# Kernel tuning notes

Hardware: AMD Instinct MI355X
Metric: run time of the kernel (lower is better)

## Reference

```python
import jax, jax.numpy as jnp
import numpy as np

N_NODES = 50000
N_EDGES = 800000
IN_CH = 128
H_CH = 128


def setup_inputs() -> dict:
    key = jax.random.key(0)
    ks = jax.random.split(key, 8)
    q = jax.random.normal(ks[0], (N_NODES, IN_CH), dtype=jnp.float32)
    k = jax.random.normal(ks[1], (N_NODES, IN_CH), dtype=jnp.float32)
    v = jax.random.normal(ks[2], (N_NODES, IN_CH), dtype=jnp.float32)
    envelope = jax.random.uniform(ks[3], (N_EDGES,), dtype=jnp.float32)
    edge_index = jax.random.randint(ks[4], (2, N_EDGES), 0, N_NODES, dtype=jnp.int64)
    # torch nn.Linear weights are [out, in]; init ~ U(-1/sqrt(fan_in), 1/sqrt(fan_in))
    s = 1.0 / np.sqrt(IN_CH)
    W_l = jax.random.uniform(ks[5], (H_CH, IN_CH), jnp.float32, -s, s)
    W_r = jax.random.uniform(ks[6], (H_CH, IN_CH), jnp.float32, -s, s)
    sa = 1.0 / np.sqrt(H_CH)
    attn_w = jax.random.uniform(ks[7], (1, H_CH), jnp.float32, -sa, sa)
    return {"q": q, "k": k, "v": v, "envelope": envelope,
            "W_l": W_l, "W_r": W_r, "attn_w": attn_w, "edge_index": edge_index}


def reference(q, k, v, envelope, W_l, W_r, attn_w, edge_index):
    # k, v are accepted but unused, matching the original module.
    N = q.shape[0]
    src = edge_index[0]
    dst = edge_index[1]
    g_l = q @ W_l.T                       # [N, H]
    g_r = q @ W_r.T                       # [N, H]
    g_l_src = g_l[src]                    # [E, H] gather
    g_sum = g_l_src + g_r[dst]            # [E, H]
    e = (jax.nn.silu(g_sum) @ attn_w.T)[:, 0]   # [E]
    e = e + jnp.log(envelope + 1e-7)
    # scatter_softmax over dst groups (numerically stable segment softmax)
    seg_max = jax.ops.segment_max(e, dst, num_segments=N)   # [N]
    ex = jnp.exp(e - seg_max[dst])                           # [E]
    denom = jax.ops.segment_sum(ex, dst, num_segments=N)     # [N]
    attn = ex / denom[dst]                                   # [E]
    out = jax.ops.segment_sum(attn[:, None] * g_l_src, dst, num_segments=N)  # [N, H]
    return out
```

## Files before the change

### kernel.cpp

```cpp
#include <hip/hip_runtime.h>
#include <math.h>

#define N_NODES 50000
#define N_EDGES 800000
#define CH 128
#define CAP 48
#define SCAT_BLOCKS ((N_EDGES + 255) / 256)
#define GEMM_BLOCKS ((N_NODES + 63) / 64)

typedef __attribute__((ext_vector_type(8))) short short8;
typedef __attribute__((ext_vector_type(4))) float f32x4;
union FragU { uint4 u; short8 s; };

__device__ __forceinline__ unsigned pack_bf16(float a, float b) {
    unsigned ua = __float_as_uint(a);
    unsigned ub = __float_as_uint(b);
    ua += 0x7FFFu + ((ua >> 16) & 1u);
    ub += 0x7FFFu + ((ub >> 16) & 1u);
    return (ua >> 16) | (ub & 0xFFFF0000u);
}

__global__ __launch_bounds__(256) void prep_pack_kernel(
    const float* __restrict__ W_l, const float* __restrict__ W_r,
    uint4* __restrict__ Wf4)
{
    int tid = blockIdx.x * 256 + threadIdx.x;
    if (tid >= 2 * 8 * 4 * 64) return;
    int lane  = tid & 63;
    int chunk = (tid >> 6) & 3;
    int tile  = (tid >> 8) & 7;
    int mat   = tid >> 11;
    const float* W = mat ? W_r : W_l;
    int n  = tile * 16 + (lane & 15);
    int k0 = chunk * 32 + (lane >> 4) * 8;
    const float* wp = W + n * CH + k0;
    float4 a = *(const float4*)wp;
    float4 b = *(const float4*)(wp + 4);
    uint4 p;
    p.x = pack_bf16(a.x, a.y);
    p.y = pack_bf16(a.z, a.w);
    p.z = pack_bf16(b.x, b.y);
    p.w = pack_bf16(b.z, b.w);
    Wf4[tid] = p;
}

__global__ __launch_bounds__(256) void fused_scatter_gemm_kernel(
    const int* __restrict__ src, const int* __restrict__ dst,
    const float* __restrict__ env,
    int* __restrict__ counts, unsigned* __restrict__ recs,
    const float* __restrict__ q, const uint4* __restrict__ Wf4,
    unsigned short* __restrict__ g_l16, float* __restrict__ g_r)
{
    const int b = blockIdx.x;
    if (b < SCAT_BLOCKS) {
        int i = b * 256 + threadIdx.x;
        if (i < N_EDGES) {
            int d = dst[i];
            int rank = atomicAdd(&counts[d], 1);
            if (rank < CAP) {
                unsigned ev = __float_as_uint(env[i] + 1e-7f);
                ev += 0x7FFFu + ((ev >> 16) & 1u);
                recs[d * CAP + rank] = (unsigned)src[i] | (ev & 0xFFFF0000u);
            }
        }
    } else {
        const int wv   = threadIdx.x >> 6;
        const int lane = threadIdx.x & 63;
        const int m    = lane & 15;
        const int quad = lane >> 4;
        const int row0 = (b - SCAT_BLOCKS) * 64 + wv * 16;

        int arow = row0 + m;
        if (arow >= N_NODES) arow = N_NODES - 1;
        const float* qr = q + (size_t)arow * CH + quad * 8;

        FragU A[4];
        #pragma unroll
        for (int c = 0; c < 4; ++c) {
            float4 x = *(const float4*)(qr + c * 32);
            float4 y = *(const float4*)(qr + c * 32 + 4);
            A[c].u.x = pack_bf16(x.x, x.y);
            A[c].u.y = pack_bf16(x.z, x.w);
            A[c].u.z = pack_bf16(y.x, y.y);
            A[c].u.w = pack_bf16(y.z, y.w);
        }

        for (int mat = 0; mat < 2; ++mat) {
            for (int tile = 0; tile < 8; ++tile) {
                f32x4 acc = {0.f, 0.f, 0.f, 0.f};
                const uint4* bp = Wf4 + (size_t)((mat * 8 + tile) * 4) * 64 + lane;
                #pragma unroll
                for (int c = 0; c < 4; ++c) {
                    FragU B; B.u = bp[c * 64];
                    acc = __builtin_amdgcn_mfma_f32_16x16x32_bf16(A[c].s, B.s, acc, 0, 0, 0);
                }
                int col = tile * 16 + m;
                #pragma unroll
                for (int r = 0; r < 4; ++r) {
                    int rowg = row0 + quad * 4 + r;
                    if (rowg < N_NODES) {
                        if (mat == 0) {
                            unsigned u = __float_as_uint(acc[r]);
                            u += 0x7FFFu + ((u >> 16) & 1u);
                            g_l16[(size_t)rowg * CH + col] = (unsigned short)(u >> 16);
                        } else {
                            g_r[(size_t)rowg * CH + col] = acc[r];
                        }
                    }
                }
            }
        }
    }
}

__global__ __launch_bounds__(256) void node_attn_kernel(
    const uint4* __restrict__ g_lb4, const float* __restrict__ g_r,
    const float* __restrict__ attn_w,
    const unsigned* __restrict__ recs, const int* __restrict__ counts,
    float* __restrict__ out)
{
    int gid = blockIdx.x * blockDim.x + threadIdx.x;
    int wid = gid >> 6;
    if (wid >= N_NODES) return;
    const int lane = threadIdx.x & 63;
    const int q4 = lane >> 4;
    const int sl = lane & 15;

    const int off = wid * CAP;
    int cnt = counts[wid];
    if (cnt > CAP) cnt = CAP;

    float gr[8], aw[8];
    {
        const float4* grp = (const float4*)(g_r + (size_t)wid * CH + sl * 8);
        float4 a = grp[0], b = grp[1];
        gr[0] = a.x; gr[1] = a.y; gr[2] = a.z; gr[3] = a.w;
        gr[4] = b.x; gr[5] = b.y; gr[6] = b.z; gr[7] = b.w;
        const float4* awp = (const float4*)(attn_w + sl * 8);
        float4 c = awp[0], d = awp[1];
        aw[0] = c.x; aw[1] = c.y; aw[2] = c.z; aw[3] = c.w;
        aw[4] = d.x; aw[5] = d.y; aw[6] = d.z; aw[7] = d.w;
    }

    float l = 0.0f;
    float acc[8] = {0.f, 0.f, 0.f, 0.f, 0.f, 0.f, 0.f, 0.f};

    if (cnt > 0) {
        int ec = min(q4, cnt - 1);
        unsigned rc = recs[off + ec];
        int   s_cur  = rc & 0xFFFFu;
        float ev_cur = __uint_as_float(rc & 0xFFFF0000u);
        uint4 g_cur  = g_lb4[(size_t)s_cur * (CH / 8) + sl];

        for (int j = 0; j < cnt; j += 4) {
            int e = j + q4;
            bool active = (e < cnt);
            int enc = min(e + 4, cnt - 1);
            unsigned rn = recs[off + enc];
            int   s_n  = rn & 0xFFFFu;
            float ev_n = __uint_as_float(rn & 0xFFFF0000u);
            uint4 g_n  = g_lb4[(size_t)s_n * (CH / 8) + sl];

            float gl[8];
            gl[0] = __uint_as_float(g_cur.x << 16);
            gl[1] = __uint_as_float(g_cur.x & 0xFFFF0000u);
            gl[2] = __uint_as_float(g_cur.y << 16);
            gl[3] = __uint_as_float(g_cur.y & 0xFFFF0000u);
            gl[4] = __uint_as_float(g_cur.z << 16);
            gl[5] = __uint_as_float(g_cur.z & 0xFFFF0000u);
            gl[6] = __uint_as_float(g_cur.w << 16);
            gl[7] = __uint_as_float(g_cur.w & 0xFFFF0000u);

            float p = 0.0f;
            #pragma unroll
            for (int c = 0; c < 8; ++c) {
                float h = gl[c] + gr[c];
                float sg = __builtin_amdgcn_rcpf(1.0f + __expf(-h));
                p = fmaf(h * aw[c], sg, p);
            }
            p += __shfl_xor(p, 1, 64);
            p += __shfl_xor(p, 2, 64);
            p += __shfl_xor(p, 4, 64);
            p += __shfl_xor(p, 8, 64);

            float w = __expf(p) * (active ? ev_cur : 0.0f);
            l += w;
            #pragma unroll
            for (int c = 0; c < 8; ++c) acc[c] = fmaf(w, gl[c], acc[c]);

            s_cur = s_n; ev_cur = ev_n; g_cur = g_n;
        }
    }

    #pragma unroll
    for (int o = 16; o <= 32; o <<= 1) {
        l += __shfl_xor(l, o, 64);
        #pragma unroll
        for (int c = 0; c < 8; ++c) acc[c] += __shfl_xor(acc[c], o, 64);
    }

    if (q4 == 0) {
        float inv = (l > 0.0f) ? __builtin_amdgcn_rcpf(l) : 0.0f;
        float4 o0 = {acc[0] * inv, acc[1] * inv, acc[2] * inv, acc[3] * inv};
        float4 o1 = {acc[4] * inv, acc[5] * inv, acc[6] * inv, acc[7] * inv};
        float4* op = (float4*)(out + (size_t)wid * CH + sl * 8);
        op[0] = o0;
        op[1] = o1;
    }
}

extern "C" void kernel_launch(void* const* d_in, const int* in_sizes, int n_in,
                              void* d_out, int out_size, void* d_ws, size_t ws_size,
                              hipStream_t stream)
{
    const float* q      = (const float*)d_in[0];
    const float* env    = (const float*)d_in[3];
    const float* W_l    = (const float*)d_in[4];
    const float* W_r    = (const float*)d_in[5];
    const float* attn_w = (const float*)d_in[6];
    const int*   eidx   = (const int*)d_in[7];
    const int* src = eidx;
    const int* dst = eidx + N_EDGES;
    float* out = (float*)d_out;

    float* ws    = (float*)d_ws;
    unsigned* g_lb = (unsigned*)ws;
    float* g_r   = (float*)(g_lb + (size_t)N_NODES * (CH / 2));
    uint4* Wf4   = (uint4*)(g_r + (size_t)N_NODES * CH);
    unsigned* recs = (unsigned*)(Wf4 + 4096);
    int* counts  = (int*)(recs + (size_t)N_NODES * CAP);

    hipMemsetAsync(counts, 0, N_NODES * sizeof(int), stream);

    prep_pack_kernel<<<16, 256, 0, stream>>>(W_l, W_r, Wf4);

    fused_scatter_gemm_kernel<<<SCAT_BLOCKS + GEMM_BLOCKS, 256, 0, stream>>>(
        src, dst, env, counts, recs, q, Wf4, (unsigned short*)g_lb, g_r);

    int node_wave_blocks = (N_NODES * 64 + 255) / 256;
    node_attn_kernel<<<node_wave_blocks, 256, 0, stream>>>(
        (const uint4*)g_lb, g_r, attn_w, recs, counts, out);
}
```

Measured before the change: 224.4 us.

## Interleave scatter and GEMM blocks and batch four edge atomics per thread

The fused scatter/GEMM launch now alternates even blocks for edge scatter and odd blocks for the projection GEMM, instead of running all scatter blocks first. The aim is to co-schedule atomic-heavy bucketing with MFMA-heavy work on the same CUs. Each scatter thread now handles four edges and issues four independent atomicAdds before writing records, which keeps more atomics in flight. In exchange there are fewer scatter threads, and edges land in each node's bucket in a different order, so the order of the per-node softmax sums can change.

```diff
diff --git a/kernel.cpp b/kernel.cpp
--- a/kernel.cpp
+++ b/kernel.cpp
@@ -5,7 +5,7 @@
 #define N_EDGES 800000
 #define CH 128
 #define CAP 48
-#define SCAT_BLOCKS ((N_EDGES + 255) / 256)
+#define SCAT_BLOCKS ((N_EDGES + 1023) / 1024)
 #define GEMM_BLOCKS ((N_NODES + 63) / 64)
 
 typedef __attribute__((ext_vector_type(8))) short short8;
@@ -52,23 +52,38 @@
     unsigned short* __restrict__ g_l16, float* __restrict__ g_r)
 {
     const int b = blockIdx.x;
-    if (b < SCAT_BLOCKS) {
-        int i = b * 256 + threadIdx.x;
-        if (i < N_EDGES) {
-            int d = dst[i];
-            int rank = atomicAdd(&counts[d], 1);
-            if (rank < CAP) {
+    if ((b & 1) == 0) {
+        const int sid = b >> 1;
+        const int i0 = sid * 1024 + threadIdx.x;
+
+        int  dd[4];
+        bool ok[4];
+        #pragma unroll
+        for (int j = 0; j < 4; ++j) {
+            int i = i0 + j * 256;
+            ok[j] = (i < N_EDGES);
+            dd[j] = ok[j] ? dst[i] : 0;
+        }
+        int rk[4];
+        #pragma unroll
+        for (int j = 0; j < 4; ++j)
+            rk[j] = ok[j] ? atomicAdd(&counts[dd[j]], 1) : CAP;
+        #pragma unroll
+        for (int j = 0; j < 4; ++j) {
+            if (ok[j] && rk[j] < CAP) {
+                int i = i0 + j * 256;
                 unsigned ev = __float_as_uint(env[i] + 1e-7f);
                 ev += 0x7FFFu + ((ev >> 16) & 1u);
-                recs[d * CAP + rank] = (unsigned)src[i] | (ev & 0xFFFF0000u);
+                recs[dd[j] * CAP + rk[j]] = (unsigned)src[i] | (ev & 0xFFFF0000u);
             }
         }
     } else {
+        const int gid  = b >> 1;
         const int wv   = threadIdx.x >> 6;
         const int lane = threadIdx.x & 63;
         const int m    = lane & 15;
         const int quad = lane >> 4;
-        const int row0 = (b - SCAT_BLOCKS) * 64 + wv * 16;
+        const int row0 = gid * 64 + wv * 16;
 
         int arow = row0 + m;
         if (arow >= N_NODES) arow = N_NODES - 1;
```

After: 233.2 us. 1.04x slower.
